# Kernel tuning notes

Hardware: AMD Instinct MI355X
Metric: run time of the kernel (lower is better)

## Reference

```python
import jax, jax.numpy as jnp
import numpy as np

H = 16  # hidden/input size
EPS = 1e-5


def _lstm_layer(xs, W_ih, W_hh, b_ih, b_hh):
    """xs: [T, B, in]. Returns (ys [T,B,H], h_final [B,H]). PyTorch gate order i,f,g,o."""
    B = xs.shape[1]
    h0 = jnp.zeros((B, H), xs.dtype)
    c0 = jnp.zeros((B, H), xs.dtype)
    bias = b_ih + b_hh  # [4H]

    def step(carry, x_t):
        h, c = carry
        gates = x_t @ W_ih.T + h @ W_hh.T + bias  # [B, 4H]
        i, f, g, o = jnp.split(gates, 4, axis=-1)
        i = jax.nn.sigmoid(i)
        f = jax.nn.sigmoid(f)
        g = jnp.tanh(g)
        o = jax.nn.sigmoid(o)
        c = f * c + i * g
        h = o * jnp.tanh(c)
        return (h, c), h

    (h_fin, _), ys = jax.lax.scan(step, (h0, c0), xs)
    return ys, h_fin


def setup_inputs() -> dict:
    key = jax.random.key(0)
    ks = jax.random.split(key, 12)
    s = 1.0 / np.sqrt(H)  # PyTorch LSTM/Linear init scale
    B, T = 4096, 512
    x = jax.random.normal(ks[0], (B, T, H), dtype=jnp.float32)
    u = lambda k, shp: jax.random.uniform(k, shp, jnp.float32, -s, s)
    return {
        "x": x,
        "W_ih0": u(ks[1], (4 * H, H)), "W_hh0": u(ks[2], (4 * H, H)),
        "b_ih0": u(ks[3], (4 * H,)), "b_hh0": u(ks[4], (4 * H,)),
        "W_ih1": u(ks[5], (4 * H, H)), "W_hh1": u(ks[6], (4 * H, H)),
        "b_ih1": u(ks[7], (4 * H,)), "b_hh1": u(ks[8], (4 * H,)),
        "W_proj": u(ks[9], (H, H)), "b_proj": u(ks[10], (H,)),
        "ln_gamma": jnp.ones((H,), jnp.float32), "ln_beta": jnp.zeros((H,), jnp.float32),
    }


def reference(x, W_ih0, W_hh0, b_ih0, b_hh0, W_ih1, W_hh1, b_ih1, b_hh1,
              W_proj, b_proj, ln_gamma, ln_beta):
    xs = jnp.transpose(x, (1, 0, 2))  # [T, B, H] time-major for scan
    ys, _ = _lstm_layer(xs, W_ih0, W_hh0, b_ih0, b_hh0)
    _, h_n = _lstm_layer(ys, W_ih1, W_hh1, b_ih1, b_hh1)  # h_n[-1] == layer-2 final h
    z = h_n @ W_proj.T + b_proj  # [B, H]
    mu = jnp.mean(z, axis=-1, keepdims=True)
    var = jnp.mean(jnp.square(z - mu), axis=-1, keepdims=True)
    z = (z - mu) * jax.lax.rsqrt(var + EPS) * ln_gamma + ln_beta
    return jnp.tanh(z)
```

## Files before the change

kernel.cpp:

```cpp
#include <hip/hip_runtime.h>
#include <cstddef>

#define HH 16
#define TT 512
#define STG 16
#define NSTG (TT / STG)
#define LOG2E 1.44269504088896340736f

typedef float v2f __attribute__((ext_vector_type(2)));
typedef float v4f __attribute__((ext_vector_type(4)));

static __device__ __forceinline__ float fexp2(float x){ return __builtin_amdgcn_exp2f(x); }
static __device__ __forceinline__ float frcp (float x){ return __builtin_amdgcn_rcpf(x); }
static __device__ __forceinline__ float frsq (float x){ return __builtin_amdgcn_rsqf(x); }

static __device__ __forceinline__ float ftanh(float c){
    return frcp(1.0f + fexp2(c * (-2.0f*LOG2E))) * 2.0f - 1.0f;
}

#if __has_builtin(__builtin_amdgcn_mov_dpp)
template<int CTRL>
static __device__ __forceinline__ float qb(float v){
    return __builtin_bit_cast(float,
        __builtin_amdgcn_mov_dpp(__builtin_bit_cast(int,v), CTRL, 0xF, 0xF, true));
}
#else
template<int CTRL>
static __device__ __forceinline__ float qb(float v){
    return __builtin_bit_cast(float,
        __builtin_amdgcn_update_dpp(0, __builtin_bit_cast(int,v), CTRL, 0xF, 0xF, true));
}
#endif

static __device__ __forceinline__ v2f pkfma(v2f a, v2f b, v2f c){
    return __builtin_elementwise_fma(a, b, c);
}

static __device__ __forceinline__ void dot16_acc(const v4f* a, const v4f* w, v2f& s0, v2f& s1){
    s0 = pkfma(a[0].lo, w[0].lo, s0);  s1 = pkfma(a[0].hi, w[0].hi, s1);
    s0 = pkfma(a[1].lo, w[1].lo, s0);  s1 = pkfma(a[1].hi, w[1].hi, s1);
    s0 = pkfma(a[2].lo, w[2].lo, s0);  s1 = pkfma(a[2].hi, w[2].hi, s1);
    s0 = pkfma(a[3].lo, w[3].lo, s0);  s1 = pkfma(a[3].hi, w[3].hi, s1);
}

static __device__ __forceinline__ void dot16_first(const v4f* a, const v4f* w, v2f bias2,
                                                   v2f& s0, v2f& s1){
    s0 = pkfma(a[0].lo, w[0].lo, bias2);
    s1 = a[0].hi * w[0].hi;
    s0 = pkfma(a[1].lo, w[1].lo, s0);  s1 = pkfma(a[1].hi, w[1].hi, s1);
    s0 = pkfma(a[2].lo, w[2].lo, s0);  s1 = pkfma(a[2].hi, w[2].hi, s1);
    s0 = pkfma(a[3].lo, w[3].lo, s0);  s1 = pkfma(a[3].hi, w[3].hi, s1);
}

static __device__ __forceinline__ void ld4(v4f* dst, const float* p){
    const v4f* q = (const v4f*)p;
    dst[0] = q[0]; dst[1] = q[1]; dst[2] = q[2]; dst[3] = q[3];
}

__global__ __launch_bounds__(256, 4) void lstm_fused_kernel(
    const float* __restrict__ x,
    const float* __restrict__ W_ih0, const float* __restrict__ W_hh0,
    const float* __restrict__ b_ih0, const float* __restrict__ b_hh0,
    const float* __restrict__ W_ih1, const float* __restrict__ W_hh1,
    const float* __restrict__ b_ih1, const float* __restrict__ b_hh1,
    const float* __restrict__ W_proj, const float* __restrict__ b_proj,
    const float* __restrict__ ln_g, const float* __restrict__ ln_b,
    float* __restrict__ out)
{
    const int lane = threadIdx.x & 63;
    const int wave = threadIdx.x >> 6;
    const int b    = blockIdx.x * 4 + wave;

    const int g   = lane & 3;
    const int k   = lane >> 2;
    const int row = g * HH + k;

    {
        const int ph = blockIdx.x & 3;
        if      (ph == 1) __builtin_amdgcn_s_sleep(2);
        else if (ph == 2) __builtin_amdgcn_s_sleep(4);
        else if (ph == 3) __builtin_amdgcn_s_sleep(6);
    }

    __shared__ float sh[4 * 544];
    float* xb0 = sh + wave * 544;
    float* xb1 = xb0 + 256;
    float* h1w = xb1 + 256;
    float* h2w = h1w + 16;

    const bool  isg   = (g == 2);
    const float sc_in = isg ? (-2.0f * LOG2E) : (-LOG2E);

    v4f wih0[4], whh0[4], wih1[4], whh1[4];
#pragma unroll
    for (int q = 0; q < 4; ++q) {
        wih0[q] = ((const v4f*)(W_ih0 + row * HH))[q] * sc_in;
        whh0[q] = ((const v4f*)(W_hh0 + row * HH))[q] * sc_in;
        wih1[q] = ((const v4f*)(W_ih1 + row * HH))[q] * sc_in;
        whh1[q] = ((const v4f*)(W_hh1 + row * HH))[q] * sc_in;
    }
    const v2f bias0v = {(b_ih0[row] + b_hh0[row]) * sc_in, 0.f};
    const v2f bias1v = {(b_ih1[row] + b_hh1[row]) * sc_in, 0.f};

    const float* xg = x + (size_t)b * TT * HH;

    v4f xs = *(const v4f*)(xg + lane * 4);
    *(v4f*)(xb0 + lane * 4) = xs;
    xs = *(const v4f*)(xg + 256 + lane * 4);

    v4f xa[4];
    ld4(xa, xb0);

    float cs1, cs2 = 0.0f;
    v4f h1a[4], h2a[4];
#pragma unroll
    for (int q = 0; q < 4; ++q) h2a[q] = (v4f)(0.f);

    {
        v2f p0, p1;
        dot16_first(xa, wih0, bias0v, p0, p1);
        v2f ps = p0 + p1;
        float a1 = ps.x + ps.y;
        float r1 = frcp(1.0f + fexp2(a1));
        float i1 = qb<0x00>(r1), g1 = qb<0xAA>(r1), o1 = qb<0xFF>(r1);
        float gs1 = __builtin_fmaf(g1, -4.0f*LOG2E, 2.0f*LOG2E);
        cs1 = i1 * gs1;
        float h1n = o1 * (frcp(1.0f + fexp2(cs1)) * 2.0f - 1.0f);
        h1w[k] = h1n;
        ld4(h1a, h1w);
        ld4(xa, xb0 + HH);
    }

    for (int s = 0; s < NSTG; ++s) {
        float* cur = (s & 1) ? xb1 : xb0;
        float* nxt = (s & 1) ? xb0 : xb1;

        *(v4f*)(nxt + lane * 4) = xs;
        const int sp = (s + 2 < NSTG) ? (s + 2) : (NSTG - 1);
        xs = *(const v4f*)(xg + (size_t)sp * 256 + lane * 4);

#pragma unroll
        for (int ti = 0; ti < STG; ++ti) {
            v2f p0, p1;
            dot16_first(xa, wih0, bias0v, p0, p1);
            dot16_acc(h1a, whh0, p0, p1);
            v2f ps = p0 + p1;
            float a1 = ps.x + ps.y;
            float r1 = frcp(1.0f + fexp2(a1));
            float i1 = qb<0x00>(r1), f1 = qb<0x55>(r1);
            float g1 = qb<0xAA>(r1), o1 = qb<0xFF>(r1);
            float gs1 = __builtin_fmaf(g1, -4.0f*LOG2E, 2.0f*LOG2E);
            cs1 = __builtin_fmaf(f1, cs1, i1 * gs1);
            float h1n = o1 * (frcp(1.0f + fexp2(cs1)) * 2.0f - 1.0f);
            h1w[k] = h1n;

            v2f q0, q1;
            dot16_first(h1a, wih1, bias1v, q0, q1);

            ld4(h1a, h1w);
            ld4(xa, (ti <= 13) ? (cur + (ti + 2) * HH) : (nxt + (ti - 14) * HH));

            dot16_acc(h2a, whh1, q0, q1);
            v2f qs = q0 + q1;
            float a2 = qs.x + qs.y;
            float r2 = frcp(1.0f + fexp2(a2));
            float i2 = qb<0x00>(r2), f2 = qb<0x55>(r2);
            float g2 = qb<0xAA>(r2), o2 = qb<0xFF>(r2);
            float gs2 = __builtin_fmaf(g2, -4.0f*LOG2E, 2.0f*LOG2E);
            cs2 = __builtin_fmaf(f2, cs2, i2 * gs2);
            float h2n = o2 * (frcp(1.0f + fexp2(cs2)) * 2.0f - 1.0f);
            h2w[k] = h2n;
            ld4(h2a, h2w);
        }
    }

    const int u = lane & 15;
    v4f wp[4];
#pragma unroll
    for (int q = 0; q < 4; ++q) wp[q] = ((const v4f*)(W_proj + u * HH))[q];
    const v2f bpv = {b_proj[u], 0.f};
    v2f z0, z1;
    dot16_first(h2a, wp, bpv, z0, z1);
    v2f zs = z0 + z1;
    float z = zs.x + zs.y;

    float sacc = z;
    sacc += __shfl_xor(sacc, 1); sacc += __shfl_xor(sacc, 2);
    sacc += __shfl_xor(sacc, 4); sacc += __shfl_xor(sacc, 8);
    const float mu = sacc * (1.0f / 16.0f);

    const float d = z - mu;
    float q2 = d * d;
    q2 += __shfl_xor(q2, 1); q2 += __shfl_xor(q2, 2);
    q2 += __shfl_xor(q2, 4); q2 += __shfl_xor(q2, 8);
    const float var = q2 * (1.0f / 16.0f);

    const float rs  = frsq(var + 1e-5f);
    const float y   = d * rs * ln_g[u] + ln_b[u];
    const float res = ftanh(y);

    if (lane < 16) out[(size_t)b * HH + lane] = res;
}

extern "C" void kernel_launch(void* const* d_in, const int* in_sizes, int n_in,
                              void* d_out, int out_size, void* d_ws, size_t ws_size,
                              hipStream_t stream) {
    const float* x      = (const float*)d_in[0];
    const float* W_ih0  = (const float*)d_in[1];
    const float* W_hh0  = (const float*)d_in[2];
    const float* b_ih0  = (const float*)d_in[3];
    const float* b_hh0  = (const float*)d_in[4];
    const float* W_ih1  = (const float*)d_in[5];
    const float* W_hh1  = (const float*)d_in[6];
    const float* b_ih1  = (const float*)d_in[7];
    const float* b_hh1  = (const float*)d_in[8];
    const float* W_proj = (const float*)d_in[9];
    const float* b_proj = (const float*)d_in[10];
    const float* ln_g   = (const float*)d_in[11];
    const float* ln_b   = (const float*)d_in[12];
    float* out = (float*)d_out;

    const int B = in_sizes[0] / (TT * HH);
    dim3 grid(B / 4), block(256);
    hipLaunchKernelGGL(lstm_fused_kernel, grid, block, 0, stream,
                       x, W_ih0, W_hh0, b_ih0, b_hh0,
                       W_ih1, W_hh1, b_ih1, b_hh1,
                       W_proj, b_proj, ln_g, ln_b, out);
}
```

Baseline: 470.6 us.

## Precompute next stage's input projection off the recurrent critical path

The layer-0 input projection x·W_ih0 + bias is now computed one stage ahead: each step of the current stage also computes one timestep of the next stage into a register array, so the dependent recurrence only does the h·W_hh0 product. The x staging buffer shrinks to a single buffer per wave. Blocks go from 4 to 8 waves, and the s_sleep stagger at kernel start is removed. The extra register arrays and the 512-thread launch bound with min 4 blocks cap the per-thread register budget much lower, which risks register spilling.

After: 487.9 us. +3.7%, slower.

```diff
diff --git a/kernel.cpp b/kernel.cpp
--- a/kernel.cpp
+++ b/kernel.cpp
@@ -5,6 +5,7 @@
 #define TT 512
 #define STG 16
 #define NSTG (TT / STG)
+#define WPB 8
 #define LOG2E 1.44269504088896340736f
 
 typedef float v2f __attribute__((ext_vector_type(2)));
@@ -57,7 +58,7 @@
     dst[0] = q[0]; dst[1] = q[1]; dst[2] = q[2]; dst[3] = q[3];
 }
 
-__global__ __launch_bounds__(256, 4) void lstm_fused_kernel(
+__global__ __launch_bounds__(512, 4) void lstm_fused_kernel(
     const float* __restrict__ x,
     const float* __restrict__ W_ih0, const float* __restrict__ W_hh0,
     const float* __restrict__ b_ih0, const float* __restrict__ b_hh0,
@@ -69,24 +70,16 @@
 {
     const int lane = threadIdx.x & 63;
     const int wave = threadIdx.x >> 6;
-    const int b    = blockIdx.x * 4 + wave;
+    const int b    = blockIdx.x * WPB + wave;
 
     const int g   = lane & 3;
     const int k   = lane >> 2;
     const int row = g * HH + k;
 
-    {
-        const int ph = blockIdx.x & 3;
-        if      (ph == 1) __builtin_amdgcn_s_sleep(2);
-        else if (ph == 2) __builtin_amdgcn_s_sleep(4);
-        else if (ph == 3) __builtin_amdgcn_s_sleep(6);
-    }
-
-    __shared__ float sh[4 * 544];
-    float* xb0 = sh + wave * 544;
-    float* xb1 = xb0 + 256;
-    float* h1w = xb1 + 256;
-    float* h2w = h1w + 16;
+    __shared__ float sh[WPB * 288];
+    float* xb  = sh + wave * 288;
+    float* h1w = xb + 256;
+    float* h2w = xb + 272;
 
     const bool  isg   = (g == 2);
     const float sc_in = isg ? (-2.0f * LOG2E) : (-LOG2E);
@@ -105,11 +98,17 @@
     const float* xg = x + (size_t)b * TT * HH;
 
     v4f xs = *(const v4f*)(xg + lane * 4);
-    *(v4f*)(xb0 + lane * 4) = xs;
+    *(v4f*)(xb + lane * 4) = xs;
     xs = *(const v4f*)(xg + 256 + lane * 4);
 
-    v4f xa[4];
-    ld4(xa, xb0);
+    float ihd[STG];
+#pragma unroll
+    for (int t = 0; t < STG; ++t) {
+        v4f xt[4]; ld4(xt, xb + t * HH);
+        v2f b0, b1; dot16_first(xt, wih0, bias0v, b0, b1);
+        v2f bs = b0 + b1;
+        ihd[t] = bs.x + bs.y;
+    }
 
     float cs1, cs2 = 0.0f;
     v4f h1a[4], h2a[4];
@@ -117,33 +116,27 @@
     for (int q = 0; q < 4; ++q) h2a[q] = (v4f)(0.f);
 
     {
-        v2f p0, p1;
-        dot16_first(xa, wih0, bias0v, p0, p1);
-        v2f ps = p0 + p1;
-        float a1 = ps.x + ps.y;
-        float r1 = frcp(1.0f + fexp2(a1));
+        float r1 = frcp(1.0f + fexp2(ihd[0]));
         float i1 = qb<0x00>(r1), g1 = qb<0xAA>(r1), o1 = qb<0xFF>(r1);
         float gs1 = __builtin_fmaf(g1, -4.0f*LOG2E, 2.0f*LOG2E);
         cs1 = i1 * gs1;
         float h1n = o1 * (frcp(1.0f + fexp2(cs1)) * 2.0f - 1.0f);
         h1w[k] = h1n;
         ld4(h1a, h1w);
-        ld4(xa, xb0 + HH);
     }
 
     for (int s = 0; s < NSTG; ++s) {
-        float* cur = (s & 1) ? xb1 : xb0;
-        float* nxt = (s & 1) ? xb0 : xb1;
-
-        *(v4f*)(nxt + lane * 4) = xs;
+        *(v4f*)(xb + lane * 4) = xs;
         const int sp = (s + 2 < NSTG) ? (s + 2) : (NSTG - 1);
         xs = *(const v4f*)(xg + (size_t)sp * 256 + lane * 4);
 
+        float ihdn[STG];
 #pragma unroll
         for (int ti = 0; ti < STG; ++ti) {
+            const float ihx = (ti <= 14) ? ihd[ti + 1] : ihdn[0];
+            const v2f  ihv = {ihx, 0.f};
             v2f p0, p1;
-            dot16_first(xa, wih0, bias0v, p0, p1);
-            dot16_acc(h1a, whh0, p0, p1);
+            dot16_first(h1a, whh0, ihv, p0, p1);
             v2f ps = p0 + p1;
             float a1 = ps.x + ps.y;
             float r1 = frcp(1.0f + fexp2(a1));
@@ -158,7 +151,8 @@
             dot16_first(h1a, wih1, bias1v, q0, q1);
 
             ld4(h1a, h1w);
-            ld4(xa, (ti <= 13) ? (cur + (ti + 2) * HH) : (nxt + (ti - 14) * HH));
+            v4f xn[4];
+            ld4(xn, xb + ti * HH);
 
             dot16_acc(h2a, whh1, q0, q1);
             v2f qs = q0 + q1;
@@ -171,7 +165,14 @@
             float h2n = o2 * (frcp(1.0f + fexp2(cs2)) * 2.0f - 1.0f);
             h2w[k] = h2n;
             ld4(h2a, h2w);
+
+            v2f b0, b1;
+            dot16_first(xn, wih0, bias0v, b0, b1);
+            v2f bs = b0 + b1;
+            ihdn[ti] = bs.x + bs.y;
         }
+#pragma unroll
+        for (int t = 0; t < STG; ++t) ihd[t] = ihdn[t];
     }
 
     const int u = lane & 15;
@@ -221,7 +222,7 @@
     float* out = (float*)d_out;
 
     const int B = in_sizes[0] / (TT * HH);
-    dim3 grid(B / 4), block(256);
+    dim3 grid(B / WPB), block(64 * WPB);
     hipLaunchKernelGGL(lstm_fused_kernel, grid, block, 0, stream,
                        x, W_ih0, W_hh0, b_ih0, b_hh0,
                        W_ih1, W_hh1, b_ih1, b_hh1,
```
